# Kernel tuning notes

Measured on AMD Instinct MI355X. Metric: run time of the kernel, lower is better.

## Reference

```python
import jax, jax.numpy as jnp
import numpy as np

NUM_HEADS = 16
CHUNK = 512


def setup_inputs() -> dict:
    key = jax.random.key(0)
    k1, k2, k3 = jax.random.split(key, 3)
    B, S, H = 2, 2048, 1024
    x = jax.random.normal(k1, (B, S, H), dtype=jnp.float32)
    w_qkv = jax.random.normal(k2, (H, 3 * H), dtype=jnp.float32) * 0.02
    b_qkv = jnp.zeros((3 * H,), dtype=jnp.float32)
    w_proj = jax.random.normal(k3, (H, H), dtype=jnp.float32) * 0.02
    b_proj = jnp.zeros((H,), dtype=jnp.float32)
    return {"x": x, "w_qkv": w_qkv, "b_qkv": b_qkv, "w_proj": w_proj, "b_proj": b_proj}


def reference(x, w_qkv, b_qkv, w_proj, b_proj):
    B, S, H = x.shape
    nh, cs = NUM_HEADS, CHUNK
    hd = H // nh
    nc = S // cs  # number of chunks (seq_len > chunk_size -> chunked branch)

    qkv = x @ w_qkv + b_qkv  # [B,S,3H]
    qkv = qkv.reshape(B, S, 3, nh, hd).transpose(2, 0, 3, 1, 4)  # [3,B,nh,S,hd]
    q, k, v = qkv[0], qkv[1], qkv[2]  # each [B,nh,S,hd]

    # split sequence into chunks: [B,nh,nc,cs,hd]
    qc = q.reshape(B, nh, nc, cs, hd)
    kc = k.reshape(B, nh, nc, cs, hd)
    vc = v.reshape(B, nh, nc, cs, hd)

    scale = 1.0 / jnp.sqrt(jnp.asarray(hd, dtype=x.dtype))
    # scores for every (q-chunk i, k-chunk j) pair: [B,nh,i,j,cs,cs]
    scores = jnp.einsum('bhicd,bhjed->bhijce', qc, kc) * scale
    # softmax is LOCAL to each k-chunk (per pair), matching the torch code
    attn = jax.nn.softmax(scores, axis=-1)
    # attend within each pair, then AVERAGE over k-chunks j
    out = jnp.einsum('bhijce,bhjed->bhicd', attn, vc) / nc  # [B,nh,nc,cs,hd]

    out = out.reshape(B, nh, S, hd).transpose(0, 2, 1, 3).reshape(B, S, H)
    # dropout is identity in eval mode
    return out @ w_proj + b_proj
```

## Files before the change

kernel.cpp:

```cpp
#include <hip/hip_runtime.h>
#include <hip/hip_bf16.h>
#include <stdint.h>

typedef __bf16 bf16;
typedef __bf16 bf16x8 __attribute__((ext_vector_type(8)));
typedef __bf16 bf16x4 __attribute__((ext_vector_type(4)));
typedef float f32x4 __attribute__((ext_vector_type(4)));

#define MFMA16(a, b, c) __builtin_amdgcn_mfma_f32_16x16x32_bf16(a, b, c, 0, 0, 0)
#define SBAR() __builtin_amdgcn_sched_barrier(0)

__device__ __forceinline__ void gload_lds16(const void* g, void* l) {
  __builtin_amdgcn_global_load_lds(
      (const __attribute__((address_space(1))) void*)g,
      (__attribute__((address_space(3))) void*)l, 16, 0, 0);
}


__global__ void f32_to_bf16_kernel(const float* __restrict__ in,
                                   bf16* __restrict__ out, int n) {
  int i = (blockIdx.x * blockDim.x + threadIdx.x) * 4;
  if (i >= n) return;
  const float4 v = *(const float4*)(in + i);
  bf16x4 o = {(bf16)v.x, (bf16)v.y, (bf16)v.z, (bf16)v.w};
  *(bf16x4*)(out + i) = o;
}

__global__ void transpose_to_bf16(const float* __restrict__ in,
                                  bf16* __restrict__ out, int R, int C) {
  __shared__ float t[32][33];
  const int tx = threadIdx.x, ty = threadIdx.y;
  const int c0 = blockIdx.x * 32, r0 = blockIdx.y * 32;
  for (int i = 0; i < 32; i += 8)
    t[ty + i][tx] = in[(size_t)(r0 + ty + i) * C + c0 + tx];
  __syncthreads();
  for (int i = 0; i < 32; i += 8)
    out[(size_t)(c0 + ty + i) * R + r0 + tx] = (bf16)t[tx][ty + i];
}

__global__ void reduce_ctx(const bf16* __restrict__ p1, bf16* __restrict__ ctx) {
  const int i = (blockIdx.x * blockDim.x + threadIdx.x) * 8;
  const bf16x8 a = *(const bf16x8*)(ctx + i);
  const bf16x8 b = *(const bf16x8*)(p1 + i);
  bf16x8 o;
#pragma unroll
  for (int j = 0; j < 8; ++j)
    o[j] = (bf16)(0.25f * ((float)a[j] + (float)b[j]));
  *(bf16x8*)(ctx + i) = o;
}


__global__ __launch_bounds__(512, 1) void gemm_qkv(
    const bf16* __restrict__ A, const bf16* __restrict__ Bt,
    const float* __restrict__ bias, bf16* __restrict__ qp,
    bf16* __restrict__ kp, bf16* __restrict__ vT) {
  __shared__ __align__(16) char lds[98304];
  const int tid = threadIdx.x;
  const int wid = tid >> 6, lane = tid & 63;
  const int l15 = lane & 15, g = lane >> 4;
  const int wr = wid >> 2, wc = wid & 3;
  const int wg = (blockIdx.x & 7) * 24 + (blockIdx.x >> 3);
  const int m0 = (wg / 12) * 256, n0 = (wg % 12) * 256;
  const int K = 1024, nt = 32;

  const int srow = tid >> 2;
  const int scol = (((tid & 3) ^ ((srow >> 1) & 3)) * 8);

  auto ldsA = [&](int bi) { return lds + bi * 32768; };
  auto ldsB = [&](int bi) { return lds + bi * 32768 + 16384; };

  auto stageA = [&](int t) {
    const int bi = t % 3, kt = t * 32;
    const bf16* s0 = A + (size_t)(m0 + srow) * K + kt + scol;
    gload_lds16(s0, ldsA(bi) + (size_t)tid * 16);
    gload_lds16(s0 + (size_t)128 * K, ldsA(bi) + 8192 + (size_t)tid * 16);
  };
  auto stageB = [&](int t) {
    const int bi = t % 3, kt = t * 32;
    const bf16* s0 = Bt + (size_t)(n0 + srow) * K + kt + scol;
    gload_lds16(s0, ldsB(bi) + (size_t)tid * 16);
    gload_lds16(s0 + (size_t)128 * K, ldsB(bi) + 8192 + (size_t)tid * 16);
  };

  f32x4 acc[8][4] = {};

  stageA(0);
  stageB(0);
  stageA(1);
  stageB(1);

  const int swzr = ((l15 >> 1) & 3) << 4;

#pragma unroll 1
  for (int t = 0; t < nt; ++t) {
    const int bi = t % 3;
    if (t < nt - 1)
      asm volatile("s_waitcnt vmcnt(4)" ::: "memory");
    else
      asm volatile("s_waitcnt vmcnt(0)" ::: "memory");
    __builtin_amdgcn_s_barrier();
    bf16x8 Bf[4], Af[4];
#pragma unroll
    for (int ni = 0; ni < 4; ++ni)
      Bf[ni] = *(const bf16x8*)(ldsB(bi) + (wc * 64 + ni * 16 + l15) * 64 +
                                ((g * 16) ^ swzr));
#pragma unroll
    for (int mi = 0; mi < 4; ++mi)
      Af[mi] = *(const bf16x8*)(ldsA(bi) + (wr * 128 + mi * 16 + l15) * 64 +
                                ((g * 16) ^ swzr));
    if (t + 2 < nt) stageA(t + 2);
    __builtin_amdgcn_s_setprio(1);
#pragma unroll
    for (int mi = 0; mi < 4; ++mi)
#pragma unroll
      for (int ni = 0; ni < 4; ++ni)
        acc[mi][ni] = MFMA16(Af[mi], Bf[ni], acc[mi][ni]);
    __builtin_amdgcn_s_setprio(0);
#pragma unroll
    for (int mi = 0; mi < 4; ++mi)
      Af[mi] = *(const bf16x8*)(ldsA(bi) +
                                (wr * 128 + 64 + mi * 16 + l15) * 64 +
                                ((g * 16) ^ swzr));
    if (t + 2 < nt) stageB(t + 2);
    __builtin_amdgcn_s_setprio(1);
#pragma unroll
    for (int mi = 0; mi < 4; ++mi)
#pragma unroll
      for (int ni = 0; ni < 4; ++ni)
        acc[4 + mi][ni] = MFMA16(Af[mi], Bf[ni], acc[4 + mi][ni]);
    __builtin_amdgcn_s_setprio(0);
  }

  const int b = m0 >> 11;
  if (n0 >= 2048) {
    __builtin_amdgcn_s_barrier();
    bf16* T = (bf16*)lds + (size_t)wid * (64 * 68);
    const int hh = (n0 - 2048 + wc * 64) >> 6;
#pragma unroll
    for (int half = 0; half < 2; ++half) {
      const int sbase = (m0 & 2047) + wr * 128 + half * 64;
#pragma unroll
      for (int ni = 0; ni < 4; ++ni) {
        const float bv = bias[n0 + wc * 64 + ni * 16 + l15];
#pragma unroll
        for (int mi = 0; mi < 4; ++mi)
#pragma unroll
          for (int rg = 0; rg < 4; ++rg)
            T[(ni * 16 + l15) * 68 + mi * 16 + g * 4 + rg] =
                (bf16)(acc[half * 4 + mi][ni][rg] + bv);
      }
      __builtin_amdgcn_s_barrier();
      bf16* vrow = vT + ((size_t)(b * 16 + hh) * 64) * 2048 + sbase;
#pragma unroll
      for (int rr = 0; rr < 16; ++rr) {
        const int d = rr * 4 + g;
        const bf16x4 v4 = *(const bf16x4*)(T + d * 68 + l15 * 4);
        *(bf16x4*)(vrow + (size_t)d * 2048 + l15 * 4) = v4;
      }
      __builtin_amdgcn_s_barrier();
    }
  } else {
    const int sec = n0 >> 10;
    bf16* dst = (sec == 0) ? qp : kp;
    const float qscale = (sec == 0) ? 0.1803368801f : 1.0f;
#pragma unroll
    for (int mi = 0; mi < 8; ++mi) {
      const int rbase = m0 + wr * 128 + mi * 16 + g * 4;
#pragma unroll
      for (int ni = 0; ni < 4; ++ni) {
        const int cc = n0 + wc * 64 + ni * 16 + l15;
        const float bv = bias[cc];
        const int hh = (cc >> 6) & 15, d = cc & 63;
#pragma unroll
        for (int rg = 0; rg < 4; ++rg) {
          const int r = rbase + rg;
          const int s = r & 2047;
          dst[((size_t)(b * 16 + hh) * 2048 + s) * 64 + d] =
              (bf16)((acc[mi][ni][rg] + bv) * qscale);
        }
      }
    }
  }
}


__global__ __launch_bounds__(256, 2) void gemm_proj(
    const bf16* __restrict__ A, const bf16* __restrict__ Bt,
    const float* __restrict__ bias, float* __restrict__ Cout, int M, int N,
    int K, int nxb) {
  __shared__ __align__(16) char smem[65536];
  const int tid = threadIdx.x;
  const int wid = tid >> 6, lane = tid & 63;
  const int l15 = lane & 15, g = lane >> 4;
  const int cpx = gridDim.x >> 3;
  const int wg = (blockIdx.x & 7) * cpx + (blockIdx.x >> 3);
  const int m0 = (wg / nxb) * 128, n0 = (wg % nxb) * 128;
  const int wr = wid >> 1, wc = wid & 1;
  const int nt = K / 64;

  const int soff = wid * 4096 + lane * 16;

  auto stage = [&](int t, int buf) {
    const int kt = t * 64;
    char* bufA = smem + buf * 32768;
    char* bufB = bufA + 16384;
#pragma unroll
    for (int c = 0; c < 4; ++c) {
      const int off = soff + c * 1024;
      const int e = off >> 1;
      const int r = e >> 6, col = e & 63;
      gload_lds16(A + (size_t)(m0 + r) * K + kt + col, bufA + off);
      gload_lds16(Bt + (size_t)(n0 + r) * K + kt + col, bufB + off);
    }
  };

  f32x4 acc[4][4] = {};

  stage(0, 0);

#pragma unroll 1
  for (int t = 0; t < nt; ++t) {
    __syncthreads();
    SBAR();
    if (t + 1 < nt) stage(t + 1, (t + 1) & 1);
    const bf16* lA = (const bf16*)(smem + (t & 1) * 32768);
    const bf16* lB = (const bf16*)(smem + (t & 1) * 32768 + 16384);
#pragma unroll
    for (int kk = 0; kk < 2; ++kk) {
      const int ko = kk * 32 + g * 8;
      bf16x8 af[4], bfr[4];
#pragma unroll
      for (int mi = 0; mi < 4; ++mi)
        af[mi] = *(const bf16x8*)(lA + (wr * 64 + mi * 16 + l15) * 64 + ko);
#pragma unroll
      for (int ni = 0; ni < 4; ++ni)
        bfr[ni] = *(const bf16x8*)(lB + (wc * 64 + ni * 16 + l15) * 64 + ko);
      __builtin_amdgcn_s_setprio(1);
#pragma unroll
      for (int mi = 0; mi < 4; ++mi)
#pragma unroll
        for (int ni = 0; ni < 4; ++ni)
          acc[mi][ni] = MFMA16(af[mi], bfr[ni], acc[mi][ni]);
      __builtin_amdgcn_s_setprio(0);
    }
  }

#pragma unroll
  for (int mi = 0; mi < 4; ++mi) {
    const int rbase = m0 + wr * 64 + mi * 16 + g * 4;
#pragma unroll
    for (int ni = 0; ni < 4; ++ni) {
      const int cc = n0 + wc * 64 + ni * 16 + l15;
      const float bv = bias[cc];
#pragma unroll
      for (int rg = 0; rg < 4; ++rg)
        Cout[(size_t)(rbase + rg) * N + cc] = acc[mi][ni][rg] + bv;
    }
  }
}


__global__ __launch_bounds__(256, 3) void attn_kernel(
    const bf16* __restrict__ qp, const bf16* __restrict__ kp,
    const bf16* __restrict__ vT, bf16* __restrict__ p0,
    bf16* __restrict__ p1) {
  __shared__ __align__(16) char lds_raw[32768 + 4 * 4608];

  const int tid = threadIdx.x;
  const int wid = tid >> 6, lane = tid & 63;
  const int l15 = lane & 15, g = lane >> 4;
  const int wg = (blockIdx.x & 7) * 128 + (blockIdx.x >> 3);
  const int ch = wg & 1, qt = (wg >> 1) & 15, bhh = wg >> 5;
  const int h = bhh & 15, b = bhh >> 4;
  const size_t bh = (size_t)bhh;
  const int rowbase = b * 2048 + qt * 128;

  bf16* Pw = (bf16*)(lds_raw + 32768 + wid * 4608);

  const bf16* qptr = qp + (bh * 2048 + (size_t)qt * 128 + wid * 32) * 64;
  bf16x8 Qf[2][2];
#pragma unroll
  for (int m = 0; m < 2; ++m)
#pragma unroll
    for (int hf = 0; hf < 2; ++hf)
      Qf[m][hf] =
          *(const bf16x8*)(qptr + (size_t)(m * 16 + l15) * 64 + hf * 32 + g * 8);

  bf16x8 ones;
#pragma unroll
  for (int i = 0; i < 8; ++i) ones[i] = (bf16)1.0f;

  const bf16* kbase = kp + bh * 2048 * 64;
  const bf16* vbase = vT + bh * 64 * 2048;

  const int srow = lane >> 3;
  const int scol = 8 * ((lane & 7) ^ srow);
  char* ldsK = lds_raw;
  char* ldsV = lds_raw + 16384;

  auto stage = [&](int tile, int buf) {
    const int r0 = wid * 16 + srow;
    const bf16* ks = kbase + ((size_t)tile * 64 + r0) * 64 + scol;
    char* kd = ldsK + buf * 8192 + wid * 2048;
    gload_lds16(ks, kd);
    gload_lds16(ks + 8 * 64, kd + 1024);
    const bf16* vs = vbase + (size_t)r0 * 2048 + tile * 64 + scol;
    char* vd = ldsV + buf * 8192 + wid * 2048;
    gload_lds16(vs, vd);
    gload_lds16(vs + 8 * 2048, vd + 1024);
  };

  f32x4 Otot[2][4] = {};
  const int swz = (l15 & 7) << 4;

  stage(ch * 16, 0);

#pragma unroll 1
  for (int c2 = 0; c2 < 2; ++c2) {
    f32x4 Och[2][4] = {};
    f32x4 ssum[2] = {};
#pragma unroll 1
    for (int h8 = 0; h8 < 8; ++h8) {
      const int t = c2 * 8 + h8;
      __syncthreads();
      SBAR();
      stage(ch * 16 + ((t + 1) & 15), (t + 1) & 1);
      const char* Kt = ldsK + (t & 1) * 8192;
      const char* Vt = ldsV + (t & 1) * 8192;
      f32x4 sacc[4][2] = {};
      __builtin_amdgcn_s_setprio(1);
#pragma unroll
      for (int t2 = 0; t2 < 4; ++t2)
#pragma unroll
        for (int hf = 0; hf < 2; ++hf) {
          const bf16x8 kf = *(const bf16x8*)(Kt + (t2 * 16 + l15) * 128 +
                                             ((hf * 64 + g * 16) ^ swz));
          sacc[t2][0] = MFMA16(Qf[0][hf], kf, sacc[t2][0]);
          sacc[t2][1] = MFMA16(Qf[1][hf], kf, sacc[t2][1]);
        }
      __builtin_amdgcn_s_setprio(0);
#pragma unroll
      for (int t2 = 0; t2 < 4; ++t2)
#pragma unroll
        for (int m = 0; m < 2; ++m)
#pragma unroll
          for (int rg = 0; rg < 4; ++rg)
            Pw[(m * 16 + g * 4 + rg) * 72 + t2 * 16 + l15] =
                (bf16)__builtin_amdgcn_exp2f(sacc[t2][m][rg]);
      __builtin_amdgcn_s_setprio(1);
#pragma unroll
      for (int kk2 = 0; kk2 < 2; ++kk2) {
        bf16x8 pa[2];
#pragma unroll
        for (int m = 0; m < 2; ++m)
          pa[m] = *(const bf16x8*)(Pw + (m * 16 + l15) * 72 + kk2 * 32 + g * 8);
#pragma unroll
        for (int n = 0; n < 4; ++n) {
          const bf16x8 vf = *(const bf16x8*)(Vt + (n * 16 + l15) * 128 +
                                             ((kk2 * 64 + g * 16) ^ swz));
          Och[0][n] = MFMA16(pa[0], vf, Och[0][n]);
          Och[1][n] = MFMA16(pa[1], vf, Och[1][n]);
        }
        ssum[0] = MFMA16(pa[0], ones, ssum[0]);
        ssum[1] = MFMA16(pa[1], ones, ssum[1]);
      }
      __builtin_amdgcn_s_setprio(0);
    }
#pragma unroll
    for (int m = 0; m < 2; ++m)
#pragma unroll
      for (int rg = 0; rg < 4; ++rg) {
        const float inv = __builtin_amdgcn_rcpf(ssum[m][rg]);
#pragma unroll
        for (int n = 0; n < 4; ++n) Otot[m][n][rg] += Och[m][n][rg] * inv;
      }
  }

  bf16* pc = ch ? p1 : p0;
#pragma unroll
  for (int m = 0; m < 2; ++m)
#pragma unroll
    for (int n = 0; n < 4; ++n)
#pragma unroll
      for (int rg = 0; rg < 4; ++rg) {
        const int r = rowbase + wid * 32 + m * 16 + g * 4 + rg;
        pc[(size_t)r * 1024 + h * 64 + n * 16 + l15] = (bf16)Otot[m][n][rg];
      }
}


extern "C" void kernel_launch(void* const* d_in, const int* in_sizes, int n_in,
                              void* d_out, int out_size, void* d_ws,
                              size_t ws_size, hipStream_t stream) {
  const float* x = (const float*)d_in[0];
  const float* w_qkv = (const float*)d_in[1];
  const float* b_qkv = (const float*)d_in[2];
  const float* w_proj = (const float*)d_in[3];
  const float* b_proj = (const float*)d_in[4];
  float* out = (float*)d_out;

  char* ws = (char*)d_ws;
  bf16* xb     = (bf16*)(ws);
  bf16* wqkvT  = (bf16*)(ws + (8u << 20));
  bf16* wprojT = (bf16*)(ws + (14u << 20));
  bf16* qp     = (bf16*)(ws + (16u << 20));
  bf16* kp     = (bf16*)(ws + (24u << 20));
  bf16* vT     = (bf16*)(ws + (32u << 20));
  bf16* ctx    = (bf16*)(ws + (40u << 20));

  hipLaunchKernelGGL(f32_to_bf16_kernel, dim3(4096), dim3(256), 0, stream, x,
                     xb, 4096 * 1024);
  hipLaunchKernelGGL(transpose_to_bf16, dim3(96, 32), dim3(32, 8), 0, stream,
                     w_qkv, wqkvT, 1024, 3072);
  hipLaunchKernelGGL(transpose_to_bf16, dim3(32, 32), dim3(32, 8), 0, stream,
                     w_proj, wprojT, 1024, 1024);
  hipLaunchKernelGGL(gemm_qkv, dim3(192), dim3(512), 0, stream, xb, wqkvT,
                     b_qkv, qp, kp, vT);
  hipLaunchKernelGGL(attn_kernel, dim3(1024), dim3(256), 0, stream, qp, kp, vT,
                     ctx, xb);
  hipLaunchKernelGGL(reduce_ctx, dim3(2048), dim3(256), 0, stream, xb, ctx);
  hipLaunchKernelGGL(gemm_proj, dim3(8 * 32), dim3(256), 0, stream, ctx,
                     wprojT, b_proj, out, 4096, 1024, 1024, 8);
}
```

Before: 118.7 us.

## Keep attention probabilities in registers via transposed QK^T MFMA, drop LDS P buffer

The QK^T MFMA now takes the key fragment as the A operand, so the score accumulator comes out transposed and its exp2 results can be packed directly into the A-operand layout of the PV MFMA. This removes the per-wave LDS round trip for P (stores, then reloads). V fragments are loaded as two 4-element halves to match the permuted k ordering. Freeing the 18 KB of P scratch lets the launch bound rise from 3 to 4 blocks per SM. The cost is more, smaller LDS reads of V and possible register pressure at the higher occupancy target.

```diff
diff --git a/kernel.cpp b/kernel.cpp
--- a/kernel.cpp
+++ b/kernel.cpp
@@ -260,11 +260,11 @@
 }
 
 
-__global__ __launch_bounds__(256, 3) void attn_kernel(
+__global__ __launch_bounds__(256, 4) void attn_kernel(
     const bf16* __restrict__ qp, const bf16* __restrict__ kp,
     const bf16* __restrict__ vT, bf16* __restrict__ p0,
     bf16* __restrict__ p1) {
-  __shared__ __align__(16) char lds_raw[32768 + 4 * 4608];
+  __shared__ __align__(16) char lds_raw[32768];
 
   const int tid = threadIdx.x;
   const int wid = tid >> 6, lane = tid & 63;
@@ -274,8 +274,6 @@
   const int h = bhh & 15, b = bhh >> 4;
   const size_t bh = (size_t)bhh;
   const int rowbase = b * 2048 + qt * 128;
-
-  bf16* Pw = (bf16*)(lds_raw + 32768 + wid * 4608);
 
   const bf16* qptr = qp + (bh * 2048 + (size_t)qt * 128 + wid * 32) * 64;
   bf16x8 Qf[2][2];
@@ -327,44 +325,45 @@
       stage(ch * 16 + ((t + 1) & 15), (t + 1) & 1);
       const char* Kt = ldsK + (t & 1) * 8192;
       const char* Vt = ldsV + (t & 1) * 8192;
-      f32x4 sacc[4][2] = {};
-      __builtin_amdgcn_s_setprio(1);
-#pragma unroll
-      for (int t2 = 0; t2 < 4; ++t2)
-#pragma unroll
-        for (int hf = 0; hf < 2; ++hf) {
-          const bf16x8 kf = *(const bf16x8*)(Kt + (t2 * 16 + l15) * 128 +
-                                             ((hf * 64 + g * 16) ^ swz));
-          sacc[t2][0] = MFMA16(Qf[0][hf], kf, sacc[t2][0]);
-          sacc[t2][1] = MFMA16(Qf[1][hf], kf, sacc[t2][1]);
+#pragma unroll
+      for (int kk2 = 0; kk2 < 2; ++kk2) {
+        f32x4 sacc[2][2] = {};
+        __builtin_amdgcn_s_setprio(1);
+#pragma unroll
+        for (int b2 = 0; b2 < 2; ++b2)
+#pragma unroll
+          for (int hf = 0; hf < 2; ++hf) {
+            const bf16x8 kf =
+                *(const bf16x8*)(Kt + ((kk2 * 2 + b2) * 16 + l15) * 128 +
+                                 ((hf * 64 + g * 16) ^ swz));
+            sacc[b2][0] = MFMA16(kf, Qf[0][hf], sacc[b2][0]);
+            sacc[b2][1] = MFMA16(kf, Qf[1][hf], sacc[b2][1]);
+          }
+        __builtin_amdgcn_s_setprio(0);
+        bf16x8 af[2];
+#pragma unroll
+        for (int m = 0; m < 2; ++m)
+#pragma unroll
+          for (int j = 0; j < 4; ++j) {
+            af[m][j] = (bf16)__builtin_amdgcn_exp2f(sacc[0][m][j]);
+            af[m][4 + j] = (bf16)__builtin_amdgcn_exp2f(sacc[1][m][j]);
+          }
+        __builtin_amdgcn_s_setprio(1);
+#pragma unroll
+        for (int n = 0; n < 4; ++n) {
+          const char* vr = Vt + (n * 16 + l15) * 128;
+          const bf16x4 lo = *(const bf16x4*)(vr + ((kk2 * 64 + g * 8) ^ swz));
+          const bf16x4 hi =
+              *(const bf16x4*)(vr + ((kk2 * 64 + 32 + g * 8) ^ swz));
+          const bf16x8 vf =
+              __builtin_shufflevector(lo, hi, 0, 1, 2, 3, 4, 5, 6, 7);
+          Och[0][n] = MFMA16(af[0], vf, Och[0][n]);
+          Och[1][n] = MFMA16(af[1], vf, Och[1][n]);
         }
-      __builtin_amdgcn_s_setprio(0);
-#pragma unroll
-      for (int t2 = 0; t2 < 4; ++t2)
-#pragma unroll
-        for (int m = 0; m < 2; ++m)
-#pragma unroll
-          for (int rg = 0; rg < 4; ++rg)
-            Pw[(m * 16 + g * 4 + rg) * 72 + t2 * 16 + l15] =
-                (bf16)__builtin_amdgcn_exp2f(sacc[t2][m][rg]);
-      __builtin_amdgcn_s_setprio(1);
-#pragma unroll
-      for (int kk2 = 0; kk2 < 2; ++kk2) {
-        bf16x8 pa[2];
-#pragma unroll
-        for (int m = 0; m < 2; ++m)
-          pa[m] = *(const bf16x8*)(Pw + (m * 16 + l15) * 72 + kk2 * 32 + g * 8);
-#pragma unroll
-        for (int n = 0; n < 4; ++n) {
-          const bf16x8 vf = *(const bf16x8*)(Vt + (n * 16 + l15) * 128 +
-                                             ((kk2 * 64 + g * 16) ^ swz));
-          Och[0][n] = MFMA16(pa[0], vf, Och[0][n]);
-          Och[1][n] = MFMA16(pa[1], vf, Och[1][n]);
-        }
-        ssum[0] = MFMA16(pa[0], ones, ssum[0]);
-        ssum[1] = MFMA16(pa[1], ones, ssum[1]);
-      }
-      __builtin_amdgcn_s_setprio(0);
+        ssum[0] = MFMA16(af[0], ones, ssum[0]);
+        ssum[1] = MFMA16(af[1], ones, ssum[1]);
+        __builtin_amdgcn_s_setprio(0);
+      }
     }
 #pragma unroll
     for (int m = 0; m < 2; ++m)
```

Measured after the change: 110.8 us. -6.6%, faster.
